# Optimization experiments

Measured on AMD Instinct MI355X. Metric: run time of the kernel, lower is better.

The kernel has to match this reference:

```python
import jax, jax.numpy as jnp
import numpy as np

ALPHA = 0.2        # LeakyReLU negative slope in EEGGraphAttentionLayer
NEG_BIG = -9e15    # zero_vec value used before softmax

B, N, F_IN, H = 32, 1024, 512, 512


def setup_inputs() -> dict:
    key = jax.random.key(0)
    k1, k2, k3, k4 = jax.random.split(key, 4)
    context = jax.random.normal(k1, (B, N, F_IN), dtype=jnp.float32)
    adj = jax.random.randint(k2, (B, N, N), 0, 2, dtype=jnp.int32)
    w = jax.random.normal(k3, (F_IN, H), dtype=jnp.float32) * (1.414 / np.sqrt(F_IN))
    a = jax.random.normal(k4, (2 * H, 1), dtype=jnp.float32) * (1.414 / np.sqrt(2 * H))
    return {"context": context, "adj": adj, "w": w, "a": a}


def reference(context, adj, w, a):
    # context: (B, N, F), adj: (B, N, N), w: (F, H), a: (2H, 1)
    # All num_pers=16 heads share the identical att module, so the mean over
    # num_pers of identical tensors equals a single application (same math).
    context = context.reshape(adj.shape[0], adj.shape[1], -1)
    Wh = jnp.einsum('bnf,fh->bnh', context, w)            # (B, N, H)
    a1, a2 = a[:H, 0], a[H:, 0]                            # (H,), (H,)
    f1 = Wh @ a1                                           # (B, N) -> source index i
    f2 = Wh @ a2                                           # (B, N) -> target index j
    # e[b,i,j] = leakyrelu(f1[b,i] + f2[b,j]); avoids the explicit N x N x 2H tensor
    e = jax.nn.leaky_relu(f1[:, :, None] + f2[:, None, :], negative_slope=ALPHA)
    e = jnp.where(adj > 0, e, NEG_BIG)
    attention = jax.nn.softmax(e, axis=-1)                 # softmax over dim=1 of (N,N)
    # F.dropout is a no-op in eval mode; epsilon=None, ctx_mask=None paths skipped.
    return jax.nn.softplus(attention)
```

## Files before the change

kernel.cpp:

```cpp
#include <hip/hip_runtime.h>
#include <math.h>

#define ALPHA 0.2f

constexpr int B = 32, N = 1024, F_IN = 512, H = 512;

typedef float f32x4 __attribute__((ext_vector_type(4)));

__global__ __launch_bounds__(64) void u_kernel(const float* __restrict__ w,
                                               const float* __restrict__ a,
                                               float* __restrict__ u) {
    const int f = blockIdx.x;
    const int l = threadIdx.x;
    const float* wrow = w + (size_t)f * H;
    float s1 = 0.f, s2 = 0.f;
#pragma unroll
    for (int it = 0; it < H / 64; ++it) {
        const int h = l + it * 64;
        const float wv = wrow[h];
        s1 += wv * a[h];
        s2 += wv * a[h + H];
    }
#pragma unroll
    for (int off = 32; off > 0; off >>= 1) {
        s1 += __shfl_xor(s1, off, 64);
        s2 += __shfl_xor(s2, off, 64);
    }
    if (l == 0) { u[f] = s1; u[f + F_IN] = s2; }
}

__global__ __launch_bounds__(256) void f_kernel(const float* __restrict__ ctx,
                                                const float* __restrict__ u,
                                                float* __restrict__ f1,
                                                float* __restrict__ f2) {
    const int wave = threadIdx.x >> 6;
    const int lane = threadIdx.x & 63;
    const int row  = blockIdx.x * 4 + wave;

    const float4* u1p = (const float4*)u;
    const float4* u2p = (const float4*)(u + F_IN);
    const float4 u1a = u1p[lane * 2],     u1b = u1p[lane * 2 + 1];
    const float4 u2a = u2p[lane * 2],     u2b = u2p[lane * 2 + 1];

    const float4* c4 = (const float4*)(ctx + (size_t)row * F_IN);
    const float4 ca = c4[lane * 2], cb = c4[lane * 2 + 1];

    float s1 = ca.x * u1a.x + ca.y * u1a.y + ca.z * u1a.z + ca.w * u1a.w
             + cb.x * u1b.x + cb.y * u1b.y + cb.z * u1b.z + cb.w * u1b.w;
    float s2 = ca.x * u2a.x + ca.y * u2a.y + ca.z * u2a.z + ca.w * u2a.w
             + cb.x * u2b.x + cb.y * u2b.y + cb.z * u2b.z + cb.w * u2b.w;

#pragma unroll
    for (int off = 32; off > 0; off >>= 1) {
        s1 += __shfl_xor(s1, off, 64);
        s2 += __shfl_xor(s2, off, 64);
    }
    if (lane == 0) { f1[row] = s1; f2[row] = s2; }
}

__device__ __forceinline__ float softplus01(float z) {
    const float z2 = z * z;
    const float t  = fmaf(z2, -5.2083335e-3f, 0.125f);
    return fmaf(z2, t, fmaf(z, 0.5f, 0.69314718f));
}

__global__ __launch_bounds__(256) void attn_kernel(const int* __restrict__ adj,
                                                   const float* __restrict__ f1,
                                                   const float* __restrict__ f2,
                                                   float* __restrict__ out) {
    const int wave = threadIdx.x >> 6;
    const int lane = threadIdx.x & 63;
    const int row0 = blockIdx.x * 8 + wave * 2;
    const int b    = row0 >> 10;

    const float4* f2b = (const float4*)(f2 + (size_t)b * N);

    int4 am[4], amn[4];
    {
        const int4* arow = (const int4*)(adj + (size_t)row0 * N);
#pragma unroll
        for (int k = 0; k < 4; ++k) am[k] = arow[k * 64 + lane];
    }

#pragma unroll
    for (int i = 0; i < 2; ++i) {
        const int row = row0 + i;
        if (i == 0) {
            const int4* arown = (const int4*)(adj + (size_t)(row0 + 1) * N);
#pragma unroll
            for (int k = 0; k < 4; ++k) amn[k] = arown[k * 64 + lane];
        }

        const float fi = f1[row];
        float p[16];
        float s = 0.f;
#pragma unroll
        for (int k = 0; k < 4; ++k) {
            const float4 fv = f2b[k * 64 + lane];
            float e0 = fi + fv.x; e0 = e0 > 0.f ? e0 : ALPHA * e0;
            float e1 = fi + fv.y; e1 = e1 > 0.f ? e1 : ALPHA * e1;
            float e2 = fi + fv.z; e2 = e2 > 0.f ? e2 : ALPHA * e2;
            float e3 = fi + fv.w; e3 = e3 > 0.f ? e3 : ALPHA * e3;
            const float q0 = (am[k].x > 0) ? __expf(e0) : 0.f;
            const float q1 = (am[k].y > 0) ? __expf(e1) : 0.f;
            const float q2 = (am[k].z > 0) ? __expf(e2) : 0.f;
            const float q3 = (am[k].w > 0) ? __expf(e3) : 0.f;
            p[k * 4 + 0] = q0; p[k * 4 + 1] = q1;
            p[k * 4 + 2] = q2; p[k * 4 + 3] = q3;
            s += (q0 + q1) + (q2 + q3);
        }

#pragma unroll
        for (int off = 32; off > 0; off >>= 1)
            s += __shfl_xor(s, off, 64);
        const float inv = (s > 0.f) ? (1.0f / s) : 0.f;

        f32x4* orow = (f32x4*)(out + (size_t)row * N);
#pragma unroll
        for (int k = 0; k < 4; ++k) {
            f32x4 o;
            o.x = softplus01(p[k * 4 + 0] * inv);
            o.y = softplus01(p[k * 4 + 1] * inv);
            o.z = softplus01(p[k * 4 + 2] * inv);
            o.w = softplus01(p[k * 4 + 3] * inv);
            __builtin_nontemporal_store(o, orow + k * 64 + lane);
        }

#pragma unroll
        for (int k = 0; k < 4; ++k) am[k] = amn[k];
    }
}

extern "C" void kernel_launch(void* const* d_in, const int* in_sizes, int n_in,
                              void* d_out, int out_size, void* d_ws, size_t ws_size,
                              hipStream_t stream) {
    const float* ctx = (const float*)d_in[0];
    const int*   adj = (const int*)d_in[1];
    const float* w   = (const float*)d_in[2];
    const float* a   = (const float*)d_in[3];
    float* out = (float*)d_out;

    float* u  = (float*)d_ws;
    float* f1 = u + 2 * F_IN;
    float* f2 = f1 + B * N;

    u_kernel<<<F_IN, 64, 0, stream>>>(w, a, u);
    f_kernel<<<(B * N) / 4, 256, 0, stream>>>(ctx, u, f1, f2);
    attn_kernel<<<(B * N) / 8, 256, 0, stream>>>(adj, f1, f2, out);
}
```

Baseline: 59.33 us.

## Pack adjacency into bitmask during projection pass, use bits in attention kernel

Reads adjacency in the projection kernel and packs it into 64-bit ballot masks stored in workspace, so the attention kernel reads a small bitmask instead of the full int32 adjacency matrix. This moves the large adjacency read into the earlier kernel alongside the context read, leaving the attention kernel mostly write-bound. It adds a mask write/read and makes the first kernel heavier; falls back to the old path if workspace is too small.

```diff
diff --git a/kernel.cpp b/kernel.cpp
--- a/kernel.cpp
+++ b/kernel.cpp
@@ -6,6 +6,8 @@
 constexpr int B = 32, N = 1024, F_IN = 512, H = 512;
 
 typedef float f32x4 __attribute__((ext_vector_type(4)));
+typedef unsigned long long u64;
+typedef u64 u64x2 __attribute__((ext_vector_type(2)));
 
 __global__ __launch_bounds__(64) void u_kernel(const float* __restrict__ w,
                                                const float* __restrict__ a,
@@ -29,10 +31,12 @@
     if (l == 0) { u[f] = s1; u[f + F_IN] = s2; }
 }
 
-__global__ __launch_bounds__(256) void f_kernel(const float* __restrict__ ctx,
-                                                const float* __restrict__ u,
-                                                float* __restrict__ f1,
-                                                float* __restrict__ f2) {
+__global__ __launch_bounds__(256) void fm_kernel(const float* __restrict__ ctx,
+                                                 const int* __restrict__ adj,
+                                                 const float* __restrict__ u,
+                                                 float* __restrict__ f1,
+                                                 float* __restrict__ f2,
+                                                 u64* __restrict__ mask) {
     const int wave = threadIdx.x >> 6;
     const int lane = threadIdx.x & 63;
     const int row  = blockIdx.x * 4 + wave;
@@ -56,6 +60,27 @@
         s2 += __shfl_xor(s2, off, 64);
     }
     if (lane == 0) { f1[row] = s1; f2[row] = s2; }
+
+    if (mask) {
+        const int4* arow = (const int4*)(adj + (size_t)row * N);
+        u64 w[16];
+#pragma unroll
+        for (int k = 0; k < 4; ++k) {
+            const int4 a4 = arow[k * 64 + lane];
+            w[k * 4 + 0] = __ballot(a4.x > 0);
+            w[k * 4 + 1] = __ballot(a4.y > 0);
+            w[k * 4 + 2] = __ballot(a4.z > 0);
+            w[k * 4 + 3] = __ballot(a4.w > 0);
+        }
+        if (lane == 0) {
+            u64x2* mp = (u64x2*)(mask + (size_t)row * 16);
+#pragma unroll
+            for (int i = 0; i < 8; ++i) {
+                u64x2 v; v.x = w[2 * i]; v.y = w[2 * i + 1];
+                mp[i] = v;
+            }
+        }
+    }
 }
 
 __device__ __forceinline__ float softplus01(float z) {
@@ -64,10 +89,60 @@
     return fmaf(z2, t, fmaf(z, 0.5f, 0.69314718f));
 }
 
-__global__ __launch_bounds__(256) void attn_kernel(const int* __restrict__ adj,
-                                                   const float* __restrict__ f1,
-                                                   const float* __restrict__ f2,
-                                                   float* __restrict__ out) {
+__global__ __launch_bounds__(256) void attn_mask_kernel(const u64* __restrict__ mask,
+                                                        const float* __restrict__ f1,
+                                                        const float* __restrict__ f2,
+                                                        float* __restrict__ out) {
+    const int wave = threadIdx.x >> 6;
+    const int lane = threadIdx.x & 63;
+    const int row  = blockIdx.x * 4 + wave;
+    const int b    = row >> 10;
+
+    const float4* f2b = (const float4*)(f2 + (size_t)b * N);
+    const u64* mrow = mask + (size_t)row * 16;
+    const float fi = f1[row];
+
+    float p[16];
+    float s = 0.f;
+#pragma unroll
+    for (int k = 0; k < 4; ++k) {
+        const float4 fv = f2b[k * 64 + lane];
+        const u64 w0 = mrow[k * 4 + 0], w1 = mrow[k * 4 + 1];
+        const u64 w2 = mrow[k * 4 + 2], w3 = mrow[k * 4 + 3];
+        float e0 = fi + fv.x; e0 = e0 > 0.f ? e0 : ALPHA * e0;
+        float e1 = fi + fv.y; e1 = e1 > 0.f ? e1 : ALPHA * e1;
+        float e2 = fi + fv.z; e2 = e2 > 0.f ? e2 : ALPHA * e2;
+        float e3 = fi + fv.w; e3 = e3 > 0.f ? e3 : ALPHA * e3;
+        const float q0 = ((w0 >> lane) & 1) ? __expf(e0) : 0.f;
+        const float q1 = ((w1 >> lane) & 1) ? __expf(e1) : 0.f;
+        const float q2 = ((w2 >> lane) & 1) ? __expf(e2) : 0.f;
+        const float q3 = ((w3 >> lane) & 1) ? __expf(e3) : 0.f;
+        p[k * 4 + 0] = q0; p[k * 4 + 1] = q1;
+        p[k * 4 + 2] = q2; p[k * 4 + 3] = q3;
+        s += (q0 + q1) + (q2 + q3);
+    }
+
+#pragma unroll
+    for (int off = 32; off > 0; off >>= 1)
+        s += __shfl_xor(s, off, 64);
+    const float inv = (s > 0.f) ? (1.0f / s) : 0.f;
+
+    f32x4* orow = (f32x4*)(out + (size_t)row * N);
+#pragma unroll
+    for (int k = 0; k < 4; ++k) {
+        f32x4 o;
+        o.x = softplus01(p[k * 4 + 0] * inv);
+        o.y = softplus01(p[k * 4 + 1] * inv);
+        o.z = softplus01(p[k * 4 + 2] * inv);
+        o.w = softplus01(p[k * 4 + 3] * inv);
+        __builtin_nontemporal_store(o, orow + k * 64 + lane);
+    }
+}
+
+__global__ __launch_bounds__(256) void attn_adj_kernel(const int* __restrict__ adj,
+                                                       const float* __restrict__ f1,
+                                                       const float* __restrict__ f2,
+                                                       float* __restrict__ out) {
     const int wave = threadIdx.x >> 6;
     const int lane = threadIdx.x & 63;
     const int row0 = blockIdx.x * 8 + wave * 2;
@@ -143,8 +218,17 @@
     float* u  = (float*)d_ws;
     float* f1 = u + 2 * F_IN;
     float* f2 = f1 + B * N;
+    u64*  mask = (u64*)(f2 + B * N);
+
+    const size_t need = (size_t)(2 * F_IN + 2 * B * N) * sizeof(float)
+                      + (size_t)B * N * 16 * sizeof(u64);
+    const bool use_mask = ws_size >= need;
 
     u_kernel<<<F_IN, 64, 0, stream>>>(w, a, u);
-    f_kernel<<<(B * N) / 4, 256, 0, stream>>>(ctx, u, f1, f2);
-    attn_kernel<<<(B * N) / 8, 256, 0, stream>>>(adj, f1, f2, out);
-}
+    fm_kernel<<<(B * N) / 4, 256, 0, stream>>>(ctx, adj, u, f1, f2,
+                                               use_mask ? mask : nullptr);
+    if (use_mask)
+        attn_mask_kernel<<<(B * N) / 4, 256, 0, stream>>>(mask, f1, f2, out);
+    else
+        attn_adj_kernel<<<(B * N) / 8, 256, 0, stream>>>(adj, f1, f2, out);
+}
```

Result: slower. 66.98 us (+12.9%).
